# Optimization experiments

Measured on AMD Instinct MI355X. Metric: run time of the kernel, lower is better.

Reference implementation:

```python
import jax, jax.numpy as jnp
import numpy as np

N = 50000      # nodes
E = 800000     # edges (avg degree 16)
F_IN = 256
F_OUT = 128
ALPHA = 0.2    # leaky-relu negative slope


def setup_inputs() -> dict:
    key = jax.random.key(0)
    k1, k2, k3, k4 = jax.random.split(key, 4)
    x = jax.random.normal(k1, (N, F_IN), dtype=jnp.float32)
    # xavier_uniform-like scale for W (gain=1.414)
    limit_w = 1.414 * np.sqrt(6.0 / (F_IN + F_OUT))
    W = jax.random.uniform(k2, (F_IN, F_OUT), dtype=jnp.float32, minval=-limit_w, maxval=limit_w)
    limit_a = 1.414 * np.sqrt(6.0 / (2 * F_OUT + 1))
    a = jax.random.uniform(k3, (2 * F_OUT, 1), dtype=jnp.float32, minval=-limit_a, maxval=limit_a)
    edge = jax.random.randint(k4, (2, E), 0, N)  # edge[0]=row/src, edge[1]=col/dst
    return {"x": x, "W": W, "a": a, "edge": edge}


def reference(x, W, a, edge):
    h = x @ W                                   # [N, F_OUT]
    src, dst = edge[0], edge[1]                 # [E], [E]
    # cat([h_i, h_j], 1) @ a == h_i @ a[:F] + h_j @ a[F:] -> compute per-node halves once
    s_src = h @ a[:F_OUT, 0]                    # [N]
    s_dst = h @ a[F_OUT:, 0]                    # [N]
    e = jax.nn.leaky_relu(s_src[src] + s_dst[dst], negative_slope=ALPHA)  # [E]
    # segment softmax over edges grouped by row (dim=1 softmax of sparse [N,N])
    m = jax.ops.segment_max(e, src, num_segments=N)       # [N], -inf for empty rows
    ex = jnp.exp(e - m[src])                               # [E]
    denom = jax.ops.segment_sum(ex, src, num_segments=N)   # [N]
    attn = ex / denom[src]                                  # [E]
    # sparse mm: h_prime[i] = sum_{edges with row i} attn * h[dst]
    h_prime = jax.ops.segment_sum(attn[:, None] * h[dst], src, num_segments=N)  # [N, F_OUT]
    return jax.nn.elu(h_prime)                  # concat=True path
```

## Files before the change

### kernel.cpp

```cpp
#include <hip/hip_runtime.h>
#include <hip/hip_bf16.h>
#include <math.h>

#define F_IN   256
#define F_OUT  128
#define ALPHA  0.2f
#define TM     64
#define DPAD   16
#define CAP    96

typedef __attribute__((ext_vector_type(8))) short s16x8;
typedef __attribute__((ext_vector_type(4))) float f32x4;
typedef __attribute__((ext_vector_type(4))) int   i32x4;

__device__ __forceinline__ ushort f2bf(float f) {
  __hip_bfloat16 h = __float2bfloat16(f);
  return *reinterpret_cast<ushort*>(&h);
}
__device__ __forceinline__ uint pk2bf(float lo, float hi) {
  return (uint)f2bf(lo) | ((uint)f2bf(hi) << 16);
}
__device__ __forceinline__ float bflo(uint u) { return __uint_as_float(u << 16); }
__device__ __forceinline__ float bfhi(uint u) { return __uint_as_float(u & 0xffff0000u); }

__global__ __launch_bounds__(256) void prep_kernel(
    const float* __restrict__ W, const float* __restrict__ avec,
    ushort* __restrict__ Wf, ushort* __restrict__ Wfs,
    int4* __restrict__ deg4, int n4, int ZB) {
  int b = blockIdx.x;
  if (b < ZB) {
    int i = b * 256 + threadIdx.x;
    if (i < n4) deg4[i] = make_int4(0, 0, 0, 0);
  } else if (b < ZB + 16) {
    int idx = (b - ZB) * 256 + threadIdx.x;
    int kb = idx >> 7, c = idx & 127;
    union { s16x8 v; ushort u[8]; } t;
#pragma unroll
    for (int j = 0; j < 8; ++j) t.u[j] = f2bf(W[(kb * 8 + j) * F_OUT + c]);
    *(s16x8*)&Wf[(size_t)idx * 8] = t.v;
  } else {
    int k = threadIdx.x;
    float s1 = 0.f, s2 = 0.f;
    for (int c = 0; c < F_OUT; ++c) {
      float wv = W[k * F_OUT + c];
      s1 += wv * avec[c];
      s2 += wv * avec[F_OUT + c];
    }
    int kb = k >> 3, j8 = k & 7;
    ushort b1 = f2bf(s1), b2 = f2bf(s2);
#pragma unroll
    for (int cc = 0; cc < 16; ++cc) {
      ushort v = (cc == 0) ? b1 : (cc == 1) ? b2 : (ushort)0;
      Wfs[((size_t)kb * 16 + cc) * 8 + j8] = v;
    }
  }
}

__global__ __launch_bounds__(256) void gemm_hist_kernel(
    const float* __restrict__ X, const ushort* __restrict__ Wf,
    const ushort* __restrict__ Wfs,
    uint* __restrict__ Hb32, float* __restrict__ s_src, float* __restrict__ s_dst,
    int M, int G,
    const int* __restrict__ src, const int* __restrict__ dst,
    int* __restrict__ degPad, int* __restrict__ colidxF, int E) {
  __shared__ __align__(16) char Xs[4][8192];
  const int tid = threadIdx.x;

  if (blockIdx.x >= G) {
    int e0 = ((blockIdx.x - G) * 256 + tid) * 4;
    if (e0 + 4 <= E) {
      i32x4 s4 = *(const i32x4*)(src + e0);
      i32x4 d4 = *(const i32x4*)(dst + e0);
      int r;
      r = atomicAdd(&degPad[(size_t)s4.x * DPAD], 1); colidxF[s4.x * CAP + r] = d4.x;
      r = atomicAdd(&degPad[(size_t)s4.y * DPAD], 1); colidxF[s4.y * CAP + r] = d4.y;
      r = atomicAdd(&degPad[(size_t)s4.z * DPAD], 1); colidxF[s4.z * CAP + r] = d4.z;
      r = atomicAdd(&degPad[(size_t)s4.w * DPAD], 1); colidxF[s4.w * CAP + r] = d4.w;
    } else {
      for (int e = e0; e < E; ++e) {
        int s = src[e];
        int r = atomicAdd(&degPad[(size_t)s * DPAD], 1);
        colidxF[s * CAP + r] = dst[e];
      }
    }
    return;
  }

  const int l = tid & 63;
  const int w = tid >> 6;
  const int lc = l & 15;
  const int lg = l >> 4;
  const int rowW = blockIdx.x * TM + w * 16;
  char* myXs = Xs[w];

  const int h = l >> 5, kbs = l & 31;
#pragma unroll
  for (int i = 0; i < 8; ++i) {
    int rr = 2 * i + h;
    int gr = rowW + rr; gr = (gr < M) ? gr : (M - 1);
    const f32x4* p = (const f32x4*)(X + (size_t)gr * F_IN + kbs * 8);
    f32x4 v0 = p[0], v1 = p[1];
    union { s16x8 vv; ushort uu[8]; } t;
    t.uu[0] = f2bf(v0[0]); t.uu[1] = f2bf(v0[1]); t.uu[2] = f2bf(v0[2]); t.uu[3] = f2bf(v0[3]);
    t.uu[4] = f2bf(v1[0]); t.uu[5] = f2bf(v1[1]); t.uu[6] = f2bf(v1[2]); t.uu[7] = f2bf(v1[3]);
    int byte = kbs * 256 + (rr ^ (kbs & 7)) * 16;
    *(s16x8*)(myXs + byte) = t.vv;
  }

  f32x4 acc[8] = {};
  f32x4 aS = {0.f, 0.f, 0.f, 0.f};
#pragma unroll
  for (int ks = 0; ks < 8; ++ks) {
    int kb = ks * 4 + lg;
    int ab = kb * 256 + (lc ^ (kb & 7)) * 16;
    s16x8 af = *(const s16x8*)(myXs + ab);
    s16x8 bS = *(const s16x8*)&Wfs[((size_t)kb * 16 + lc) * 8];
#pragma unroll
    for (int j = 0; j < 8; ++j) {
      s16x8 bj = *(const s16x8*)&Wf[((size_t)kb * F_OUT + j * 16 + lc) * 8];
      acc[j] = __builtin_amdgcn_mfma_f32_16x16x32_bf16(af, bj, acc[j], 0, 0, 0);
    }
    aS = __builtin_amdgcn_mfma_f32_16x16x32_bf16(af, bS, aS, 0, 0, 0);
  }

#pragma unroll
  for (int q = 0; q < 4; ++q) {
    int rg = rowW + lg * 4 + q;
    if (rg < M) {
#pragma unroll
      for (int j = 0; j < 4; ++j)
        Hb32[(size_t)rg * 64 + j * 16 + lc] = pk2bf(acc[j][q], acc[j + 4][q]);
    }
  }

  if (lc < 2) {
    float* sout = (lc == 0) ? s_src : s_dst;
#pragma unroll
    for (int q = 0; q < 4; ++q) {
      int rg = rowW + lg * 4 + q;
      if (rg < M) sout[rg] = aS[q];
    }
  }
}

__global__ __launch_bounds__(256) void aggregate_kernel(
    const uint* __restrict__ H32, const float* __restrict__ s_src,
    const float* __restrict__ s_dst, const int* __restrict__ degPad,
    const int* __restrict__ colidxF, float* __restrict__ out, int M) {
  int node = blockIdx.x * 4 + (threadIdx.x >> 6);
  int l = threadIdx.x & 63;
  if (node >= M) return;
  const int g = l >> 4;
  const int lc = l & 15;
  int deg = degPad[(size_t)node * DPAD];
  if (deg > CAP) deg = CAP;
  const int base0 = node * CAP;
  float ssrc = s_src[node];
  float m = -INFINITY, denom = 0.f;
  float acc[8] = {};

  for (int base = 0; base < deg; base += 64) {
    int cnt = deg - base; if (cnt > 64) cnt = 64;
    int jv = 0; float ev = -INFINITY;
    if (l < cnt) {
      jv = colidxF[base0 + base + l];
      float e = ssrc + s_dst[jv];
      ev = (e > 0.f) ? e : ALPHA * e;
    }
    float cm = ev;
#pragma unroll
    for (int mask = 1; mask < 64; mask <<= 1) cm = fmaxf(cm, __shfl_xor(cm, mask));
    float mn = fmaxf(m, cm);
    float wv = (l < cnt) ? __expf(ev - mn) : 0.f;
    float sw = wv;
#pragma unroll
    for (int mask = 1; mask < 64; mask <<= 1) sw += __shfl_xor(sw, mask);
    float resc = __expf(m - mn);
    denom = denom * resc + sw;
#pragma unroll
    for (int t = 0; t < 8; ++t) acc[t] *= resc;
    m = mn;

    for (int k = 0; k < cnt; k += 8) {
      int k0 = k + g, k1 = k + 4 + g;
      int j0 = __shfl(jv, k0);
      int j1 = (k1 < 64) ? __shfl(jv, k1) : 0;
      float w0 = __shfl(wv, k0);
      float w1 = (k1 < 64) ? __shfl(wv, k1) : 0.f;
      uint4 u0 = *(const uint4*)(H32 + ((size_t)(uint)j0 << 6) + lc * 4);
      uint4 u1 = *(const uint4*)(H32 + ((size_t)(uint)j1 << 6) + lc * 4);
      acc[0] += w0 * bflo(u0.x) + w1 * bflo(u1.x);
      acc[1] += w0 * bfhi(u0.x) + w1 * bfhi(u1.x);
      acc[2] += w0 * bflo(u0.y) + w1 * bflo(u1.y);
      acc[3] += w0 * bfhi(u0.y) + w1 * bfhi(u1.y);
      acc[4] += w0 * bflo(u0.z) + w1 * bflo(u1.z);
      acc[5] += w0 * bfhi(u0.z) + w1 * bfhi(u1.z);
      acc[6] += w0 * bflo(u0.w) + w1 * bflo(u1.w);
      acc[7] += w0 * bfhi(u0.w) + w1 * bfhi(u1.w);
    }
  }

#pragma unroll
  for (int t = 0; t < 8; ++t) {
    acc[t] += __shfl_xor(acc[t], 16);
    acc[t] += __shfl_xor(acc[t], 32);
  }
  float inv = (denom > 0.f) ? 1.f / denom : 0.f;
  if (g == 0) {
    float4 v;
    v.x = acc[0] * inv; v.y = acc[2] * inv; v.z = acc[4] * inv; v.w = acc[6] * inv;
    v.x = (v.x > 0.f) ? v.x : __expf(v.x) - 1.f;
    v.y = (v.y > 0.f) ? v.y : __expf(v.y) - 1.f;
    v.z = (v.z > 0.f) ? v.z : __expf(v.z) - 1.f;
    v.w = (v.w > 0.f) ? v.w : __expf(v.w) - 1.f;
    *(float4*)&out[(size_t)node * 128 + lc * 4] = v;
  } else if (g == 1) {
    float4 v;
    v.x = acc[1] * inv; v.y = acc[3] * inv; v.z = acc[5] * inv; v.w = acc[7] * inv;
    v.x = (v.x > 0.f) ? v.x : __expf(v.x) - 1.f;
    v.y = (v.y > 0.f) ? v.y : __expf(v.y) - 1.f;
    v.z = (v.z > 0.f) ? v.z : __expf(v.z) - 1.f;
    v.w = (v.w > 0.f) ? v.w : __expf(v.w) - 1.f;
    *(float4*)&out[(size_t)node * 128 + 64 + lc * 4] = v;
  }
}

extern "C" void kernel_launch(void* const* d_in, const int* in_sizes, int n_in,
                              void* d_out, int out_size, void* d_ws, size_t ws_size,
                              hipStream_t stream) {
  const float* x    = (const float*)d_in[0];
  const float* W    = (const float*)d_in[1];
  const float* avec = (const float*)d_in[2];
  const int*   edge = (const int*)d_in[3];

  const int M = in_sizes[0] / F_IN;
  const int E = in_sizes[3] / 2;
  const int* src = edge;
  const int* dst = edge + E;
  float* out = (float*)d_out;

  char* ws = (char*)d_ws;
  uint*   Hb32    = (uint*)ws;   ws += (size_t)M * 64 * sizeof(uint);
  ushort* Wf      = (ushort*)ws; ws += (size_t)32 * F_OUT * 8 * sizeof(ushort);
  ushort* Wfs     = (ushort*)ws; ws += (size_t)32 * 16 * 8 * sizeof(ushort);
  float*  s_src   = (float*)ws;  ws += (size_t)M * sizeof(float);
  float*  s_dst   = (float*)ws;  ws += (size_t)M * sizeof(float);
  int*    degPad  = (int*)ws;    ws += (size_t)M * DPAD * sizeof(int);
  int*    colidxF = (int*)ws;    ws += (size_t)M * CAP * sizeof(int);

  const int n4 = M * DPAD / 4;
  const int ZB = (n4 + 255) / 256;
  const int E4 = (E + 1023) / 1024;
  const int G  = (M + TM - 1) / TM;

  prep_kernel<<<ZB + 17, 256, 0, stream>>>(W, avec, Wf, Wfs, (int4*)degPad, n4, ZB);
  gemm_hist_kernel<<<G + E4, 256, 0, stream>>>(x, Wf, Wfs, Hb32, s_src, s_dst,
                                               M, G, src, dst, degPad, colidxF, E);
  aggregate_kernel<<<(M + 3) / 4, 256, 0, stream>>>(Hb32, s_src, s_dst, degPad, colidxF, out, M);
}
```

Measured before the change: 93.03 us.

## Pre-convert X to bf16 in prep kernel and load tiles via global_load_lds

Moves the fp32-to-bf16 conversion of X out of the GEMM kernel into extra blocks of the prep kernel, which write a bf16 copy of X to workspace. The GEMM kernel then streams swizzled bf16 tiles directly into LDS with global_load_lds, avoiding register staging and conversion ALU work. This adds a full extra write and re-read of a bf16 copy of X through global memory, increasing total memory traffic.

New measurement: 97.11 us. +4.4%, slower.

```diff
diff --git a/kernel.cpp b/kernel.cpp
--- a/kernel.cpp
+++ b/kernel.cpp
@@ -23,9 +23,16 @@
 __device__ __forceinline__ float bflo(uint u) { return __uint_as_float(u << 16); }
 __device__ __forceinline__ float bfhi(uint u) { return __uint_as_float(u & 0xffff0000u); }
 
+__device__ __forceinline__ void gload_lds16(const void* g, void* l) {
+  __builtin_amdgcn_global_load_lds(
+      (const __attribute__((address_space(1))) void*)g,
+      (__attribute__((address_space(3))) void*)l, 16, 0, 0);
+}
+
 __global__ __launch_bounds__(256) void prep_kernel(
     const float* __restrict__ W, const float* __restrict__ avec,
-    ushort* __restrict__ Wf, ushort* __restrict__ Wfs,
+    const float* __restrict__ X,
+    ushort* __restrict__ Wf, ushort* __restrict__ Wfs, ushort* __restrict__ Xb,
     int4* __restrict__ deg4, int n4, int ZB) {
   int b = blockIdx.x;
   if (b < ZB) {
@@ -38,7 +45,7 @@
 #pragma unroll
     for (int j = 0; j < 8; ++j) t.u[j] = f2bf(W[(kb * 8 + j) * F_OUT + c]);
     *(s16x8*)&Wf[(size_t)idx * 8] = t.v;
-  } else {
+  } else if (b == ZB + 16) {
     int k = threadIdx.x;
     float s1 = 0.f, s2 = 0.f;
     for (int c = 0; c < F_OUT; ++c) {
@@ -53,11 +60,19 @@
       ushort v = (cc == 0) ? b1 : (cc == 1) ? b2 : (ushort)0;
       Wfs[((size_t)kb * 16 + cc) * 8 + j8] = v;
     }
+  } else {
+    size_t idx = ((size_t)(b - ZB - 17) * 256 + threadIdx.x) * 8;
+    const f32x4* p = (const f32x4*)(X + idx);
+    f32x4 v0 = p[0], v1 = p[1];
+    union { s16x8 vv; ushort uu[8]; } t;
+    t.uu[0] = f2bf(v0[0]); t.uu[1] = f2bf(v0[1]); t.uu[2] = f2bf(v0[2]); t.uu[3] = f2bf(v0[3]);
+    t.uu[4] = f2bf(v1[0]); t.uu[5] = f2bf(v1[1]); t.uu[6] = f2bf(v1[2]); t.uu[7] = f2bf(v1[3]);
+    *(s16x8*)&Xb[idx] = t.vv;
   }
 }
 
 __global__ __launch_bounds__(256) void gemm_hist_kernel(
-    const float* __restrict__ X, const ushort* __restrict__ Wf,
+    const ushort* __restrict__ Xb, const ushort* __restrict__ Wf,
     const ushort* __restrict__ Wfs,
     uint* __restrict__ Hb32, float* __restrict__ s_src, float* __restrict__ s_dst,
     int M, int G,
@@ -93,19 +108,15 @@
   const int rowW = blockIdx.x * TM + w * 16;
   char* myXs = Xs[w];
 
-  const int h = l >> 5, kbs = l & 31;
 #pragma unroll
   for (int i = 0; i < 8; ++i) {
-    int rr = 2 * i + h;
+    int kbs = i * 4 + lg;
+    int rr = lc ^ (kbs & 7);
     int gr = rowW + rr; gr = (gr < M) ? gr : (M - 1);
-    const f32x4* p = (const f32x4*)(X + (size_t)gr * F_IN + kbs * 8);
-    f32x4 v0 = p[0], v1 = p[1];
-    union { s16x8 vv; ushort uu[8]; } t;
-    t.uu[0] = f2bf(v0[0]); t.uu[1] = f2bf(v0[1]); t.uu[2] = f2bf(v0[2]); t.uu[3] = f2bf(v0[3]);
-    t.uu[4] = f2bf(v1[0]); t.uu[5] = f2bf(v1[1]); t.uu[6] = f2bf(v1[2]); t.uu[7] = f2bf(v1[3]);
-    int byte = kbs * 256 + (rr ^ (kbs & 7)) * 16;
-    *(s16x8*)(myXs + byte) = t.vv;
-  }
+    const char* gp = (const char*)Xb + (size_t)gr * 512 + kbs * 16;
+    gload_lds16(gp, myXs + i * 1024);
+  }
+  asm volatile("s_waitcnt vmcnt(0)" ::: "memory");
 
   f32x4 acc[8] = {};
   f32x4 aS = {0.f, 0.f, 0.f, 0.f};
@@ -247,14 +258,17 @@
   float*  s_dst   = (float*)ws;  ws += (size_t)M * sizeof(float);
   int*    degPad  = (int*)ws;    ws += (size_t)M * DPAD * sizeof(int);
   int*    colidxF = (int*)ws;    ws += (size_t)M * CAP * sizeof(int);
+  ushort* Xb      = (ushort*)ws; ws += (size_t)M * F_IN * sizeof(ushort);
 
   const int n4 = M * DPAD / 4;
   const int ZB = (n4 + 255) / 256;
+  const int CB = (M * F_IN / 8 + 255) / 256;
   const int E4 = (E + 1023) / 1024;
   const int G  = (M + TM - 1) / TM;
 
-  prep_kernel<<<ZB + 17, 256, 0, stream>>>(W, avec, Wf, Wfs, (int4*)degPad, n4, ZB);
-  gemm_hist_kernel<<<G + E4, 256, 0, stream>>>(x, Wf, Wfs, Hb32, s_src, s_dst,
+  prep_kernel<<<ZB + 17 + CB, 256, 0, stream>>>(W, avec, x, Wf, Wfs, Xb,
+                                                (int4*)degPad, n4, ZB);
+  gemm_hist_kernel<<<G + E4, 256, 0, stream>>>(Xb, Wf, Wfs, Hb32, s_src, s_dst,
                                                M, G, src, dst, degPad, colidxF, E);
   aggregate_kernel<<<(M + 3) / 4, 256, 0, stream>>>(Hb32, s_src, s_dst, degPad, colidxF, out, M);
 }
```
